# Kernel optimization log

Measured on AMD Instinct MI355X. Metric: run time of the kernel, lower is better.

Reference implementation:

```python
import jax, jax.numpy as jnp
import numpy as np

N = 50000        # nodes
E = 1600000      # edges (avg degree 32)
CZ = 64          # c_z pair channel dim
STEPS = 3        # num_equilibration_steps
DITHER = 1e-4    # dither_eps in average_rotations


def quat_mul(a, b):
    # Hamilton product, quats as [w, x, y, z]
    aw, ax, ay, az = a[..., 0], a[..., 1], a[..., 2], a[..., 3]
    bw, bx, by, bz = b[..., 0], b[..., 1], b[..., 2], b[..., 3]
    return jnp.stack([
        aw * bw - ax * bx - ay * by - az * bz,
        aw * bx + ax * bw + ay * bz - az * by,
        aw * by - ax * bz + ay * bw + az * bx,
        aw * bz + ax * by - ay * bx + az * bw,
    ], axis=-1)


def quat_conj(q):
    return q * jnp.array([1.0, -1.0, -1.0, -1.0], q.dtype)


def quat_to_rot(q):
    w, x, y, z = q[..., 0], q[..., 1], q[..., 2], q[..., 3]
    r00 = 1 - 2 * (y * y + z * z); r01 = 2 * (x * y - w * z); r02 = 2 * (x * z + w * y)
    r10 = 2 * (x * y + w * z); r11 = 1 - 2 * (x * x + z * z); r12 = 2 * (y * z - w * x)
    r20 = 2 * (x * z - w * y); r21 = 2 * (y * z + w * x); r22 = 1 - 2 * (x * x + y * y)
    return jnp.stack([
        jnp.stack([r00, r01, r02], -1),
        jnp.stack([r10, r11, r12], -1),
        jnp.stack([r20, r21, r22], -1),
    ], axis=-2)


def rotmat_to_quat(R):
    # Branchless Shepperd method: 4 candidates, pick numerically best.
    m00, m01, m02 = R[..., 0, 0], R[..., 0, 1], R[..., 0, 2]
    m10, m11, m12 = R[..., 1, 0], R[..., 1, 1], R[..., 1, 2]
    m20, m21, m22 = R[..., 2, 0], R[..., 2, 1], R[..., 2, 2]
    q0 = jnp.stack([1 + m00 + m11 + m22, m21 - m12, m02 - m20, m10 - m01], -1)
    q1 = jnp.stack([m21 - m12, 1 + m00 - m11 - m22, m01 + m10, m02 + m20], -1)
    q2 = jnp.stack([m02 - m20, m01 + m10, 1 - m00 + m11 - m22, m12 + m21], -1)
    q3 = jnp.stack([m10 - m01, m02 + m20, m12 + m21, 1 - m00 - m11 + m22], -1)
    cand = jnp.stack([q0, q1, q2, q3], axis=-2)           # [N,4,4]
    scores = jnp.stack([m00 + m11 + m22, m00, m11, m22], -1)
    idx = jnp.argmax(scores, axis=-1)
    q = cand[jnp.arange(cand.shape[0]), idx]              # [N,4]
    q = q / jnp.linalg.norm(q, axis=-1, keepdims=True)
    return q * jnp.where(q[..., :1] < 0, -1.0, 1.0)      # canonical w >= 0


def rotmat_to_rotvec(R):
    q = rotmat_to_quat(R)
    w, v = q[..., 0], q[..., 1:]
    vn = jnp.linalg.norm(v, axis=-1)
    theta = 2.0 * jnp.arctan2(vn, w)
    small = vn < 1e-6
    safe = jnp.where(small, 1.0, vn)
    return jnp.where(small[..., None], 2.0 * v, (theta / safe)[..., None] * v)


def rotvec_to_quat(rotvec, eps=1e-8):
    theta = jnp.linalg.norm(rotvec + eps, axis=-1)
    omega = rotvec / theta[..., None]
    return jnp.concatenate([jnp.cos(theta / 2)[..., None],
                            jnp.sin(theta / 2)[..., None] * omega], axis=-1)


def setup_inputs() -> dict:
    key = jax.random.key(0)
    ks = jax.random.split(key, 8)
    return {
        "edge_features": jax.random.normal(ks[0], (E, CZ), jnp.float32),
        "quats": jax.random.normal(ks[1], (N, 4), jnp.float32),
        "trans": jax.random.normal(ks[2], (N, 3), jnp.float32) * 10.0,
        "W_update": jax.random.normal(ks[3], (CZ, 6), jnp.float32) * 0.02,
        "b_update": jax.random.normal(ks[4], (6,), jnp.float32) * 0.02,
        "W_logits": jax.random.normal(ks[5], (CZ, 1), jnp.float32) * 0.1,
        "b_logits": jax.random.normal(ks[6], (1,), jnp.float32) * 0.1,
        "edge_index": jax.random.randint(ks[7], (2, E), 0, N, jnp.int32),
    }


def reference(edge_features, quats, trans, W_update, b_update, W_logits, b_logits, edge_index):
    n = quats.shape[0]
    dst, src = edge_index[0], edge_index[1]

    # pairwise update vec + segment softmax weights over destination node (edge_index[1])
    q_upd = edge_features @ W_update + b_update              # [E,6]
    logits = edge_features @ W_logits + b_logits             # [E,1]
    seg_max = jax.ops.segment_max(logits, src, num_segments=n)
    seg_max = jnp.where(jnp.isfinite(seg_max), seg_max, 0.0)
    ex = jnp.exp(logits - seg_max[src])
    denom = jax.ops.segment_sum(ex, src, num_segments=n)
    weights = ex / (denom[src] + 1e-16)                      # [E,1]

    # relative rigid: inv(dst) o src
    qn = quats / jnp.linalg.norm(quats, axis=-1, keepdims=True)
    Rn = quat_to_rot(qn)                                     # [N,3,3]
    q_rel = quat_mul(quat_conj(qn[dst]), qn[src])            # [E,4]
    t_rel = jnp.einsum('eji,ej->ei', Rn[dst], trans[src] - trans[dst])  # R^T (t_s - t_d)

    # compose_q_update_vec (openfold): q' = q + q*(0,b,c,d), normalized; t' = t + R(q) t_vec
    bcd, tvec = q_upd[:, :3], q_upd[:, 3:]
    pair_q = q_rel + quat_mul(q_rel, jnp.concatenate([jnp.zeros_like(bcd[:, :1]), bcd], -1))
    pair_q = pair_q / jnp.linalg.norm(pair_q, axis=-1, keepdims=True)
    pair_t = t_rel + jnp.einsum('eij,ej->ei', quat_to_rot(q_rel), tvec)
    pair_R = quat_to_rot(pair_q)                             # [E,3,3]

    # equilibrate loop: scatter rotation averaging with SVD projection
    R, t = Rn, trans
    key = jax.random.key(42)
    for step in range(STEPS):
        dst_R, dst_t = R[dst], t[dst]
        R_pred = jnp.einsum('eij,ejk->eik', dst_R, pair_R)   # [E,3,3]
        R_sum = jax.ops.segment_sum((R_pred * weights[:, :, None]).reshape(-1, 9),
                                    src, num_segments=n).reshape(n, 3, 3)
        R_sum = R_sum + DITHER * jax.random.normal(jax.random.fold_in(key, step),
                                                   R_sum.shape, R_sum.dtype)
        U, S, Vh = jnp.linalg.svd(R_sum, full_matrices=False)
        d = jnp.linalg.det(U @ Vh)
        col = jnp.stack([jnp.ones_like(d), jnp.ones_like(d), d], -1)[:, None, :]
        R = U @ (Vh * col)                                   # proper rotation
        t_pred = dst_t + jnp.einsum('eij,ej->ei', dst_R, pair_t)
        t = jax.ops.segment_sum(t_pred * weights, src, num_segments=n)

    q_out = rotvec_to_quat(rotmat_to_rotvec(R))
    return jnp.concatenate([q_out, t], axis=-1)              # [N,7]
```

## Files before the change

### kernel.cpp

```cpp
#include <hip/hip_runtime.h>
#include <math.h>

#define TPB 256
#define SCAN_B 1024

__device__ __forceinline__ void quat_to_R(float w, float x, float y, float z, float* R) {
    R[0] = 1.f - 2.f*(y*y + z*z);
    R[1] = 2.f*(x*y - w*z);
    R[2] = 2.f*(x*z + w*y);
    R[3] = 2.f*(x*y + w*z);
    R[4] = 1.f - 2.f*(x*x + z*z);
    R[5] = 2.f*(y*z - w*x);
    R[6] = 2.f*(x*z - w*y);
    R[7] = 2.f*(y*z + w*x);
    R[8] = 1.f - 2.f*(x*x + y*y);
}

__device__ __forceinline__ float hsum32(float v) {
    #pragma unroll
    for (int o = 16; o > 0; o >>= 1) v += __shfl_xor(v, o);
    return v;
}
__device__ __forceinline__ float hmax32(float v) {
    #pragma unroll
    for (int o = 16; o > 0; o >>= 1) v = fmaxf(v, __shfl_xor(v, o));
    return v;
}

__global__ __launch_bounds__(TPB) void k_init(
    const float* __restrict__ quats, const float* __restrict__ trans,
    float* __restrict__ qn, float* __restrict__ RT, int* __restrict__ deg, int N)
{
    int n = blockIdx.x * TPB + threadIdx.x;
    if (n >= N) return;
    float4 q = ((const float4*)quats)[n];
    float inv = rsqrtf(q.x*q.x + q.y*q.y + q.z*q.z + q.w*q.w);
    float w = q.x*inv, x = q.y*inv, y = q.z*inv, z = q.w*inv;
    ((float4*)qn)[n] = make_float4(w, x, y, z);
    float R[9];
    quat_to_R(w, x, y, z, R);
    float t0 = trans[(size_t)n*3+0], t1 = trans[(size_t)n*3+1], t2 = trans[(size_t)n*3+2];
    float4* rt = (float4*)(RT + (size_t)n*12);
    rt[0] = make_float4(R[0], R[1], R[2], t0);
    rt[1] = make_float4(R[3], R[4], R[5], t1);
    rt[2] = make_float4(R[6], R[7], R[8], t2);
    deg[n] = 0;
}

__global__ __launch_bounds__(TPB) void k_hist(
    const int* __restrict__ ei, int* __restrict__ deg, int E)
{
    int e = blockIdx.x * TPB + threadIdx.x;
    if (e >= E) return;
    atomicAdd(deg + ei[(size_t)E + e], 1);
}

__global__ __launch_bounds__(SCAN_B) void k_scan1(
    const int* __restrict__ deg, int* __restrict__ row, int* __restrict__ bsum, int N)
{
    __shared__ int sh[SCAN_B];
    int i = blockIdx.x * SCAN_B + threadIdx.x;
    int v = (i < N) ? deg[i] : 0;
    sh[threadIdx.x] = v;
    __syncthreads();
    #pragma unroll
    for (int o = 1; o < SCAN_B; o <<= 1) {
        int t = (threadIdx.x >= o) ? sh[threadIdx.x - o] : 0;
        __syncthreads();
        sh[threadIdx.x] += t;
        __syncthreads();
    }
    if (i < N) row[i] = sh[threadIdx.x] - v;
    if (threadIdx.x == SCAN_B - 1) bsum[blockIdx.x] = sh[SCAN_B - 1];
}

__global__ __launch_bounds__(SCAN_B) void k_scan2(int* __restrict__ bsum, int nb)
{
    __shared__ int sh[SCAN_B];
    int v = (threadIdx.x < nb) ? bsum[threadIdx.x] : 0;
    sh[threadIdx.x] = v;
    __syncthreads();
    #pragma unroll
    for (int o = 1; o < SCAN_B; o <<= 1) {
        int t = (threadIdx.x >= o) ? sh[threadIdx.x - o] : 0;
        __syncthreads();
        sh[threadIdx.x] += t;
        __syncthreads();
    }
    if (threadIdx.x < nb) bsum[threadIdx.x] = sh[threadIdx.x] - v;
}

__global__ __launch_bounds__(TPB) void k_scan3(
    int* __restrict__ row, const int* __restrict__ bsum,
    int* __restrict__ cursor, int N, int E)
{
    int i = blockIdx.x * TPB + threadIdx.x;
    if (i >= N) return;
    int v = row[i] + bsum[i >> 10];
    row[i] = v;
    cursor[i] = v;
    if (i == 0) row[N] = E;
}

__global__ __launch_bounds__(TPB) void k_edge_pre(
    const float* __restrict__ ef, const int* __restrict__ ei,
    const float* __restrict__ qn, const float* __restrict__ trans,
    const float* __restrict__ Wu, const float* __restrict__ bu,
    const float* __restrict__ Wl, const float* __restrict__ bl,
    int* __restrict__ cursor, float4* __restrict__ pay, int E)
{
    __shared__ __align__(16) float Ws[7][64];
    for (int i = threadIdx.x; i < 7*64; i += TPB) {
        int j = i >> 6, k = i & 63;
        Ws[j][k] = (j < 6) ? Wu[k*6 + j] : Wl[k];
    }
    __syncthreads();
    int t = blockIdx.x * TPB + threadIdx.x;
    int e = t >> 2, sub = t & 3;
    if (e >= E) return;

    float acc[7] = {0.f,0.f,0.f,0.f,0.f,0.f,0.f};
    const float4* ef4 = (const float4*)(ef + (size_t)e * 64) + sub * 4;
    #pragma unroll
    for (int k = 0; k < 4; ++k) {
        float4 v = ef4[k];
        #pragma unroll
        for (int j = 0; j < 7; ++j) {
            float4 w = ((const float4*)Ws[j])[sub*4 + k];
            acc[j] = fmaf(v.x, w.x, fmaf(v.y, w.y, fmaf(v.z, w.z, fmaf(v.w, w.w, acc[j]))));
        }
    }
    #pragma unroll
    for (int j = 0; j < 7; ++j) {
        acc[j] += __shfl_xor(acc[j], 1);
        acc[j] += __shfl_xor(acc[j], 2);
    }
    if (sub) return;

    #pragma unroll
    for (int j = 0; j < 6; ++j) acc[j] += bu[j];
    acc[6] += bl[0];

    int dst = ei[e];
    int src = ei[(size_t)E + e];
    float4 qd = ((const float4*)qn)[dst];
    float4 qs = ((const float4*)qn)[src];
    float aw = qd.x, ax = -qd.y, ay = -qd.z, az = -qd.w;
    float bw = qs.x, bx = qs.y, by = qs.z, bz = qs.w;
    float rw = aw*bw - ax*bx - ay*by - az*bz;
    float rx = aw*bx + ax*bw + ay*bz - az*by;
    float ry = aw*by - ax*bz + ay*bw + az*bx;
    float rz = aw*bz + ax*by - ay*bx + az*bw;
    float b0 = acc[0], b1 = acc[1], b2 = acc[2];
    float pw = rw - rx*b0 - ry*b1 - rz*b2;
    float px = rx + rw*b0 + ry*b2 - rz*b1;
    float py = ry + rw*b1 - rx*b2 + rz*b0;
    float pz = rz + rw*b2 + rx*b1 - ry*b0;
    float pinv = rsqrtf(pw*pw + px*px + py*py + pz*pz);
    pw *= pinv; px *= pinv; py *= pinv; pz *= pinv;
    float dx = trans[(size_t)src*3+0] - trans[(size_t)dst*3+0];
    float dy = trans[(size_t)src*3+1] - trans[(size_t)dst*3+1];
    float dz = trans[(size_t)src*3+2] - trans[(size_t)dst*3+2];
    float Rd[9];
    quat_to_R(qd.x, qd.y, qd.z, qd.w, Rd);
    float tr0 = Rd[0]*dx + Rd[3]*dy + Rd[6]*dz;
    float tr1 = Rd[1]*dx + Rd[4]*dy + Rd[7]*dz;
    float tr2 = Rd[2]*dx + Rd[5]*dy + Rd[8]*dz;
    float Rr[9];
    quat_to_R(rw, rx, ry, rz, Rr);
    float t3 = acc[3], t4 = acc[4], t5 = acc[5];
    float pt0 = tr0 + Rr[0]*t3 + Rr[1]*t4 + Rr[2]*t5;
    float pt1 = tr1 + Rr[3]*t3 + Rr[4]*t4 + Rr[5]*t5;
    float pt2 = tr2 + Rr[6]*t3 + Rr[7]*t4 + Rr[8]*t5;

    int pos = atomicAdd(cursor + src, 1);
    unsigned ub = (unsigned)dst | (pw < 0.f ? 0x80000000u : 0u);
    pay[2*(size_t)pos+0] = make_float4(px, py, pz, __uint_as_float(ub));
    pay[2*(size_t)pos+1] = make_float4(pt0, pt1, pt2, acc[6]);
}

__global__ __launch_bounds__(TPB) void k_node_softmax(
    const int* __restrict__ row, float4* __restrict__ pay, int N)
{
    int g = blockIdx.x * TPB + threadIdx.x;
    int node = g >> 5;
    int ln = threadIdx.x & 31;
    if (node >= N) return;
    int start = row[node], end = row[node + 1];
    float m = -INFINITY, s = 0.f;
    for (int i = start + ln; i < end; i += 32) {
        float l = pay[2*(size_t)i+1].w;
        float mn = fmaxf(m, l);
        s = s * expf(m - mn) + expf(l - mn);
        m = mn;
    }
    float M = hmax32(m);
    float sadj = (m == -INFINITY) ? 0.f : s * expf(m - M);
    float S = hsum32(sadj);
    float inv = 1.f / (S + 1e-16f);
    for (int i = start + ln; i < end; i += 32) {
        float4 v = pay[2*(size_t)i+1];
        v.w = expf(v.w - M) * inv;
        pay[2*(size_t)i+1] = v;
    }
}

__global__ __launch_bounds__(TPB) void k_node_iter(
    const int* __restrict__ row, const float4* __restrict__ pay,
    const float* __restrict__ RT, float* __restrict__ RS, int N)
{
    int g = blockIdx.x * TPB + threadIdx.x;
    int node = g >> 5;
    int ln = threadIdx.x & 31;
    if (node >= N) return;
    int start = row[node], end = row[node + 1];

    float a00=0,a01=0,a02=0,a10=0,a11=0,a12=0,a20=0,a21=0,a22=0,s0=0,s1=0,s2=0;
    for (int i = start + ln; i < end; i += 32) {
        float4 q  = pay[2*(size_t)i+0];
        float4 tl = pay[2*(size_t)i+1];
        unsigned ub = __float_as_uint(q.w);
        int dst = (int)(ub & 0x7fffffffu);
        float s2q = q.x*q.x + q.y*q.y + q.z*q.z;
        float pw = sqrtf(fmaxf(0.f, 1.f - s2q));
        if (ub & 0x80000000u) pw = -pw;
        float w = tl.w;
        float P[9];
        quat_to_R(pw, q.x, q.y, q.z, P);
        const float4* rt = (const float4*)(RT + (size_t)dst * 12);
        float4 r0 = rt[0], r1 = rt[1], r2 = rt[2];
        a00 += w * (r0.x*P[0] + r0.y*P[3] + r0.z*P[6]);
        a01 += w * (r0.x*P[1] + r0.y*P[4] + r0.z*P[7]);
        a02 += w * (r0.x*P[2] + r0.y*P[5] + r0.z*P[8]);
        a10 += w * (r1.x*P[0] + r1.y*P[3] + r1.z*P[6]);
        a11 += w * (r1.x*P[1] + r1.y*P[4] + r1.z*P[7]);
        a12 += w * (r1.x*P[2] + r1.y*P[5] + r1.z*P[8]);
        a20 += w * (r2.x*P[0] + r2.y*P[3] + r2.z*P[6]);
        a21 += w * (r2.x*P[1] + r2.y*P[4] + r2.z*P[7]);
        a22 += w * (r2.x*P[2] + r2.y*P[5] + r2.z*P[8]);
        s0 += w * (r0.w + r0.x*tl.x + r0.y*tl.y + r0.z*tl.z);
        s1 += w * (r1.w + r1.x*tl.x + r1.y*tl.y + r1.z*tl.z);
        s2 += w * (r2.w + r2.x*tl.x + r2.y*tl.y + r2.z*tl.z);
    }
    a00 = hsum32(a00); a01 = hsum32(a01); a02 = hsum32(a02);
    a10 = hsum32(a10); a11 = hsum32(a11); a12 = hsum32(a12);
    a20 = hsum32(a20); a21 = hsum32(a21); a22 = hsum32(a22);
    s0 = hsum32(s0); s1 = hsum32(s1); s2 = hsum32(s2);
    if (ln == 0) {
        float4* rs = (float4*)(RS + (size_t)node * 12);
        rs[0] = make_float4(a00, a01, a02, s0);
        rs[1] = make_float4(a10, a11, a12, s1);
        rs[2] = make_float4(a20, a21, a22, s2);
    }
}

#define JROT(SPP,SQQ,SPQ,SPR,SQR, VP0,VP1,VP2, VQ0,VQ1,VQ2) do { \
    float apq_ = SPQ; \
    if (fabsf(apq_) > 1e-30f) { \
        float tau_ = (SQQ - SPP) / (2.0f * apq_); \
        float tt_ = copysignf(1.0f, tau_) / (fabsf(tau_) + sqrtf(1.0f + tau_*tau_)); \
        float c_ = 1.0f / sqrtf(1.0f + tt_*tt_); \
        float s_ = tt_ * c_; \
        SPP -= tt_ * apq_; SQQ += tt_ * apq_; SPQ = 0.0f; \
        float pr_ = SPR, qr_ = SQR; \
        SPR = c_*pr_ - s_*qr_; SQR = s_*pr_ + c_*qr_; \
        float a_, b_; \
        a_ = VP0; b_ = VQ0; VP0 = c_*a_ - s_*b_; VQ0 = s_*a_ + c_*b_; \
        a_ = VP1; b_ = VQ1; VP1 = c_*a_ - s_*b_; VQ1 = s_*a_ + c_*b_; \
        a_ = VP2; b_ = VQ2; VP2 = c_*a_ - s_*b_; VQ2 = s_*a_ + c_*b_; \
    } \
} while (0)

#define CSW(LA,LB, A0,A1,A2, B0,B1,B2) do { \
    if (LB > LA) { float t_; \
        t_=LA; LA=LB; LB=t_; \
        t_=A0; A0=B0; B0=t_; \
        t_=A1; A1=B1; B1=t_; \
        t_=A2; A2=B2; B2=t_; } \
} while (0)

__global__ __launch_bounds__(TPB) void k_node_project(
    float* __restrict__ RT, const float* __restrict__ RS, int N)
{
    int n = blockIdx.x * TPB + threadIdx.x;
    if (n >= N) return;
    const float4* rs = (const float4*)(RS + (size_t)n * 12);
    float4 q0 = rs[0], q1 = rs[1], q2 = rs[2];
    float A[9] = {q0.x, q0.y, q0.z, q1.x, q1.y, q1.z, q2.x, q2.y, q2.z};
    float t0 = q0.w, t1 = q1.w, t2 = q2.w;

    float s00 = A[0]*A[0] + A[3]*A[3] + A[6]*A[6];
    float s11 = A[1]*A[1] + A[4]*A[4] + A[7]*A[7];
    float s22 = A[2]*A[2] + A[5]*A[5] + A[8]*A[8];
    float s01 = A[0]*A[1] + A[3]*A[4] + A[6]*A[7];
    float s02 = A[0]*A[2] + A[3]*A[5] + A[6]*A[8];
    float s12 = A[1]*A[2] + A[4]*A[5] + A[7]*A[8];
    float v00=1.f,v01=0.f,v02=0.f, v10=0.f,v11=1.f,v12=0.f, v20=0.f,v21=0.f,v22=1.f;
    #pragma unroll
    for (int sweep = 0; sweep < 8; ++sweep) {
        JROT(s00,s11,s01, s02,s12, v00,v10,v20, v01,v11,v21);
        JROT(s00,s22,s02, s01,s12, v00,v10,v20, v02,v12,v22);
        JROT(s11,s22,s12, s01,s02, v01,v11,v21, v02,v12,v22);
    }
    CSW(s00,s11, v00,v10,v20, v01,v11,v21);
    CSW(s00,s22, v00,v10,v20, v02,v12,v22);
    CSW(s11,s22, v01,v11,v21, v02,v12,v22);

    float u0x = A[0]*v00 + A[1]*v10 + A[2]*v20;
    float u0y = A[3]*v00 + A[4]*v10 + A[5]*v20;
    float u0z = A[6]*v00 + A[7]*v10 + A[8]*v20;
    float n0 = sqrtf(u0x*u0x + u0y*u0y + u0z*u0z);
    if (n0 > 1e-20f) { float r = 1.0f/n0; u0x*=r; u0y*=r; u0z*=r; }
    else { u0x = 1.f; u0y = 0.f; u0z = 0.f; }
    float u1x = A[0]*v01 + A[1]*v11 + A[2]*v21;
    float u1y = A[3]*v01 + A[4]*v11 + A[5]*v21;
    float u1z = A[6]*v01 + A[7]*v11 + A[8]*v21;
    float d01 = u1x*u0x + u1y*u0y + u1z*u0z;
    u1x -= d01*u0x; u1y -= d01*u0y; u1z -= d01*u0z;
    float n1 = sqrtf(u1x*u1x + u1y*u1y + u1z*u1z);
    if (n1 > 1e-12f) { float r = 1.0f/n1; u1x*=r; u1y*=r; u1z*=r; }
    else {
        float hx = (fabsf(u0x) < 0.9f) ? 1.f : 0.f;
        float hy = 1.f - hx;
        float cx = -u0z*hy, cy = u0z*hx, cz = u0x*hy - u0y*hx;
        float cn = rsqrtf(cx*cx + cy*cy + cz*cz);
        u1x = cx*cn; u1y = cy*cn; u1z = cz*cn;
    }
    float u2x = u0y*u1z - u0z*u1y;
    float u2y = u0z*u1x - u0x*u1z;
    float u2z = u0x*u1y - u0y*u1x;
    float detV = v00*(v11*v22 - v12*v21) - v01*(v10*v22 - v12*v20) + v02*(v10*v21 - v11*v20);
    if (detV < 0.f) { v02 = -v02; v12 = -v12; v22 = -v22; }
    float4* rt = (float4*)(RT + (size_t)n * 12);
    rt[0] = make_float4(u0x*v00 + u1x*v01 + u2x*v02,
                        u0x*v10 + u1x*v11 + u2x*v12,
                        u0x*v20 + u1x*v21 + u2x*v22, t0);
    rt[1] = make_float4(u0y*v00 + u1y*v01 + u2y*v02,
                        u0y*v10 + u1y*v11 + u2y*v12,
                        u0y*v20 + u1y*v21 + u2y*v22, t1);
    rt[2] = make_float4(u0z*v00 + u1z*v01 + u2z*v02,
                        u0z*v10 + u1z*v11 + u2z*v12,
                        u0z*v20 + u1z*v21 + u2z*v22, t2);
}

__global__ __launch_bounds__(TPB) void k_finalize(
    const float* __restrict__ RT, float* __restrict__ out, int N)
{
    int n = blockIdx.x * TPB + threadIdx.x;
    if (n >= N) return;
    const float4* rt = (const float4*)(RT + (size_t)n * 12);
    float4 r0 = rt[0], r1 = rt[1], r2 = rt[2];
    float m00 = r0.x, m01 = r0.y, m02 = r0.z;
    float m10 = r1.x, m11 = r1.y, m12 = r1.z;
    float m20 = r2.x, m21 = r2.y, m22 = r2.z;
    float tr = m00 + m11 + m22;
    int idx = 0; float best = tr;
    if (m00 > best) { best = m00; idx = 1; }
    if (m11 > best) { best = m11; idx = 2; }
    if (m22 > best) { best = m22; idx = 3; }
    float qw, qx, qy, qz;
    if (idx == 0)      { qw = 1.f+m00+m11+m22; qx = m21-m12;        qy = m02-m20;        qz = m10-m01; }
    else if (idx == 1) { qw = m21-m12;         qx = 1.f+m00-m11-m22; qy = m01+m10;       qz = m02+m20; }
    else if (idx == 2) { qw = m02-m20;         qx = m01+m10;        qy = 1.f-m00+m11-m22; qz = m12+m21; }
    else               { qw = m10-m01;         qx = m02+m20;        qy = m12+m21;        qz = 1.f-m00-m11+m22; }
    float inv = rsqrtf(qw*qw + qx*qx + qy*qy + qz*qz);
    qw *= inv; qx *= inv; qy *= inv; qz *= inv;
    if (qw < 0.f) { qw = -qw; qx = -qx; qy = -qy; qz = -qz; }
    float vn = sqrtf(qx*qx + qy*qy + qz*qz);
    float theta = 2.f * atan2f(vn, qw);
    float r0v, r1v, r2v;
    if (vn < 1e-6f) { r0v = 2.f*qx; r1v = 2.f*qy; r2v = 2.f*qz; }
    else { float s = theta / vn; r0v = s*qx; r1v = s*qy; r2v = s*qz; }
    float e0 = r0v + 1e-8f, e1 = r1v + 1e-8f, e2 = r2v + 1e-8f;
    float th2 = sqrtf(e0*e0 + e1*e1 + e2*e2);
    float half = 0.5f * th2;
    float cw = cosf(half), sw = sinf(half);
    float it = 1.0f / th2;
    out[(size_t)n*7+0] = cw;
    out[(size_t)n*7+1] = sw * r0v * it;
    out[(size_t)n*7+2] = sw * r1v * it;
    out[(size_t)n*7+3] = sw * r2v * it;
    out[(size_t)n*7+4] = r0.w;
    out[(size_t)n*7+5] = r1.w;
    out[(size_t)n*7+6] = r2.w;
}

extern "C" void kernel_launch(void* const* d_in, const int* in_sizes, int n_in,
                              void* d_out, int out_size, void* d_ws, size_t ws_size,
                              hipStream_t stream)
{
    (void)n_in; (void)out_size; (void)ws_size;
    const float* ef    = (const float*)d_in[0];
    const float* quats = (const float*)d_in[1];
    const float* trans = (const float*)d_in[2];
    const float* Wu    = (const float*)d_in[3];
    const float* bu    = (const float*)d_in[4];
    const float* Wl    = (const float*)d_in[5];
    const float* bl    = (const float*)d_in[6];
    const int*   ei    = (const int*)d_in[7];
    float* out = (float*)d_out;

    const int N = in_sizes[1] / 4;
    const int E = in_sizes[7] / 2;

    float* ws = (float*)d_ws;
    size_t off = 0;
    float*  qn   = ws + off; off += (size_t)4*N;
    float4* pay  = (float4*)(ws + off); off += (size_t)8*E;
    float*  RT   = ws + off; off += (size_t)12*N;
    float*  RS   = ws + off; off += (size_t)12*N;
    int* deg    = (int*)(ws + off); off += (size_t)N;
    int* row    = (int*)(ws + off); off += (size_t)(N + 1);
    int* bsum   = (int*)(ws + off); off += (size_t)SCAN_B;

    int nodeBlocks = (N + TPB - 1) / TPB;
    int edgeBlocks = (E + TPB - 1) / TPB;
    int edge4Blocks = (int)(((size_t)4*E + TPB - 1) / TPB);
    int halfBlocks = (int)(((size_t)N * 32 + TPB - 1) / TPB);
    int scanBlocks = (N + SCAN_B - 1) / SCAN_B;

    k_init<<<nodeBlocks, TPB, 0, stream>>>(quats, trans, qn, RT, deg, N);
    k_hist<<<edgeBlocks, TPB, 0, stream>>>(ei, deg, E);
    k_scan1<<<scanBlocks, SCAN_B, 0, stream>>>(deg, row, bsum, N);
    k_scan2<<<1, SCAN_B, 0, stream>>>(bsum, scanBlocks);
    k_scan3<<<nodeBlocks, TPB, 0, stream>>>(row, bsum, deg, N, E);
    k_edge_pre<<<edge4Blocks, TPB, 0, stream>>>(ef, ei, qn, trans, Wu, bu, Wl, bl,
                                                deg, pay, E);
    k_node_softmax<<<halfBlocks, TPB, 0, stream>>>(row, pay, N);
    for (int s = 0; s < 3; ++s) {
        k_node_iter<<<halfBlocks, TPB, 0, stream>>>(row, pay, RT, RS, N);
        k_node_project<<<nodeBlocks, TPB, 0, stream>>>(RT, RS, N);
    }
    k_finalize<<<nodeBlocks, TPB, 0, stream>>>(RT, out, N);
}
```

Baseline: 365.3 us.

## Decouple CSR scatter from edge precompute via index permutation and gather in softmax

Edge precompute now writes its 32-byte payload in edge order, and a separate kernel builds a CSR permutation index with atomics. The softmax kernel gathers the payloads through that index and writes them CSR-ordered into a second buffer. This removes the scattered atomic-position writes from the heavy edge kernel so its stores are coalesced. In exchange it adds an extra kernel, an extra full payload copy (read plus write of about 51 MB) and an E-sized index buffer.

After: 495.1 us. 35.5% more time.

```diff
diff --git a/kernel.cpp b/kernel.cpp
--- a/kernel.cpp
+++ b/kernel.cpp
@@ -102,12 +102,22 @@
     if (i == 0) row[N] = E;
 }
 
+__global__ __launch_bounds__(TPB) void k_scatter_idx(
+    const int* __restrict__ ei, int* __restrict__ cursor, int* __restrict__ idx, int E)
+{
+    int e = blockIdx.x * TPB + threadIdx.x;
+    if (e >= E) return;
+    int src = ei[(size_t)E + e];
+    int pos = atomicAdd(cursor + src, 1);
+    idx[pos] = e;
+}
+
 __global__ __launch_bounds__(TPB) void k_edge_pre(
     const float* __restrict__ ef, const int* __restrict__ ei,
     const float* __restrict__ qn, const float* __restrict__ trans,
     const float* __restrict__ Wu, const float* __restrict__ bu,
     const float* __restrict__ Wl, const float* __restrict__ bl,
-    int* __restrict__ cursor, float4* __restrict__ pay, int E)
+    float4* __restrict__ payE, int E)
 {
     __shared__ __align__(16) float Ws[7][64];
     for (int i = threadIdx.x; i < 7*64; i += TPB) {
@@ -173,23 +183,25 @@
     float pt1 = tr1 + Rr[3]*t3 + Rr[4]*t4 + Rr[5]*t5;
     float pt2 = tr2 + Rr[6]*t3 + Rr[7]*t4 + Rr[8]*t5;
 
-    int pos = atomicAdd(cursor + src, 1);
     unsigned ub = (unsigned)dst | (pw < 0.f ? 0x80000000u : 0u);
-    pay[2*(size_t)pos+0] = make_float4(px, py, pz, __uint_as_float(ub));
-    pay[2*(size_t)pos+1] = make_float4(pt0, pt1, pt2, acc[6]);
+    payE[2*(size_t)e+0] = make_float4(px, py, pz, __uint_as_float(ub));
+    payE[2*(size_t)e+1] = make_float4(pt0, pt1, pt2, acc[6]);
 }
 
 __global__ __launch_bounds__(TPB) void k_node_softmax(
-    const int* __restrict__ row, float4* __restrict__ pay, int N)
+    const int* __restrict__ row, const int* __restrict__ idx,
+    const float4* __restrict__ payE, float4* __restrict__ payC, int N)
 {
     int g = blockIdx.x * TPB + threadIdx.x;
     int node = g >> 5;
     int ln = threadIdx.x & 31;
     if (node >= N) return;
     int start = row[node], end = row[node + 1];
+    const float* pf = (const float*)payE;
     float m = -INFINITY, s = 0.f;
     for (int i = start + ln; i < end; i += 32) {
-        float l = pay[2*(size_t)i+1].w;
+        int e = idx[i];
+        float l = pf[8*(size_t)e + 7];
         float mn = fmaxf(m, l);
         s = s * expf(m - mn) + expf(l - mn);
         m = mn;
@@ -199,14 +211,17 @@
     float S = hsum32(sadj);
     float inv = 1.f / (S + 1e-16f);
     for (int i = start + ln; i < end; i += 32) {
-        float4 v = pay[2*(size_t)i+1];
-        v.w = expf(v.w - M) * inv;
-        pay[2*(size_t)i+1] = v;
+        int e = idx[i];
+        float4 a = payE[2*(size_t)e+0];
+        float4 b = payE[2*(size_t)e+1];
+        b.w = expf(b.w - M) * inv;
+        payC[2*(size_t)i+0] = a;
+        payC[2*(size_t)i+1] = b;
     }
 }
 
 __global__ __launch_bounds__(TPB) void k_node_iter(
-    const int* __restrict__ row, const float4* __restrict__ pay,
+    const int* __restrict__ row, const float4* __restrict__ payC,
     const float* __restrict__ RT, float* __restrict__ RS, int N)
 {
     int g = blockIdx.x * TPB + threadIdx.x;
@@ -217,8 +232,8 @@
 
     float a00=0,a01=0,a02=0,a10=0,a11=0,a12=0,a20=0,a21=0,a22=0,s0=0,s1=0,s2=0;
     for (int i = start + ln; i < end; i += 32) {
-        float4 q  = pay[2*(size_t)i+0];
-        float4 tl = pay[2*(size_t)i+1];
+        float4 q  = payC[2*(size_t)i+0];
+        float4 tl = payC[2*(size_t)i+1];
         unsigned ub = __float_as_uint(q.w);
         int dst = (int)(ub & 0x7fffffffu);
         float s2q = q.x*q.x + q.y*q.y + q.z*q.z;
@@ -406,12 +421,14 @@
     float* ws = (float*)d_ws;
     size_t off = 0;
     float*  qn   = ws + off; off += (size_t)4*N;
-    float4* pay  = (float4*)(ws + off); off += (size_t)8*E;
+    float4* payE = (float4*)(ws + off); off += (size_t)8*E;
+    float4* payC = (float4*)(ws + off); off += (size_t)8*E;
     float*  RT   = ws + off; off += (size_t)12*N;
     float*  RS   = ws + off; off += (size_t)12*N;
     int* deg    = (int*)(ws + off); off += (size_t)N;
     int* row    = (int*)(ws + off); off += (size_t)(N + 1);
     int* bsum   = (int*)(ws + off); off += (size_t)SCAN_B;
+    int* idx    = (int*)(ws + off); off += (size_t)E;
 
     int nodeBlocks = (N + TPB - 1) / TPB;
     int edgeBlocks = (E + TPB - 1) / TPB;
@@ -424,11 +441,12 @@
     k_scan1<<<scanBlocks, SCAN_B, 0, stream>>>(deg, row, bsum, N);
     k_scan2<<<1, SCAN_B, 0, stream>>>(bsum, scanBlocks);
     k_scan3<<<nodeBlocks, TPB, 0, stream>>>(row, bsum, deg, N, E);
+    k_scatter_idx<<<edgeBlocks, TPB, 0, stream>>>(ei, deg, idx, E);
     k_edge_pre<<<edge4Blocks, TPB, 0, stream>>>(ef, ei, qn, trans, Wu, bu, Wl, bl,
-                                                deg, pay, E);
-    k_node_softmax<<<halfBlocks, TPB, 0, stream>>>(row, pay, N);
+                                                payE, E);
+    k_node_softmax<<<halfBlocks, TPB, 0, stream>>>(row, idx, payE, payC, N);
     for (int s = 0; s < 3; ++s) {
-        k_node_iter<<<halfBlocks, TPB, 0, stream>>>(row, pay, RT, RS, N);
+        k_node_iter<<<halfBlocks, TPB, 0, stream>>>(row, payC, RT, RS, N);
         k_node_project<<<nodeBlocks, TPB, 0, stream>>>(RT, RS, N);
     }
     k_finalize<<<nodeBlocks, TPB, 0, stream>>>(RT, out, N);
```

## Split edge GEMV from geometry kernel and interleave edge feature loads

Applied to the files above, without the earlier changes.

Splits the fused edge preprocessing kernel into a 4-threads-per-edge projection kernel writing two float4 intermediates, and a 1-thread-per-edge geometry kernel that does quaternion math, the cursor atomic, and payload scatter. The feature load pattern changes so the four sub-threads read adjacent float4s, improving coalescing. Previously 3 of 4 lanes idled during geometry. The cost is an extra kernel launch and a round trip of 32 bytes per edge through global memory.

Result: slower. 389.1 us (+6.5%).

```diff
diff --git a/kernel.cpp b/kernel.cpp
--- a/kernel.cpp
+++ b/kernel.cpp
@@ -102,12 +102,11 @@
     if (i == 0) row[N] = E;
 }
 
-__global__ __launch_bounds__(TPB) void k_edge_pre(
-    const float* __restrict__ ef, const int* __restrict__ ei,
-    const float* __restrict__ qn, const float* __restrict__ trans,
+__global__ __launch_bounds__(TPB) void k_gemm(
+    const float* __restrict__ ef,
     const float* __restrict__ Wu, const float* __restrict__ bu,
     const float* __restrict__ Wl, const float* __restrict__ bl,
-    int* __restrict__ cursor, float4* __restrict__ pay, int E)
+    float4* __restrict__ qa, float4* __restrict__ qb, int E)
 {
     __shared__ __align__(16) float Ws[7][64];
     for (int i = threadIdx.x; i < 7*64; i += TPB) {
@@ -120,13 +119,13 @@
     if (e >= E) return;
 
     float acc[7] = {0.f,0.f,0.f,0.f,0.f,0.f,0.f};
-    const float4* ef4 = (const float4*)(ef + (size_t)e * 64) + sub * 4;
+    const float4* ef4 = (const float4*)(ef + (size_t)e * 64);
     #pragma unroll
     for (int k = 0; k < 4; ++k) {
-        float4 v = ef4[k];
+        float4 v = ef4[sub + 4*k];
         #pragma unroll
         for (int j = 0; j < 7; ++j) {
-            float4 w = ((const float4*)Ws[j])[sub*4 + k];
+            float4 w = ((const float4*)Ws[j])[sub + 4*k];
             acc[j] = fmaf(v.x, w.x, fmaf(v.y, w.y, fmaf(v.z, w.z, fmaf(v.w, w.w, acc[j]))));
         }
     }
@@ -136,11 +135,20 @@
         acc[j] += __shfl_xor(acc[j], 2);
     }
     if (sub) return;
-
-    #pragma unroll
-    for (int j = 0; j < 6; ++j) acc[j] += bu[j];
-    acc[6] += bl[0];
-
+    qa[e] = make_float4(acc[0] + bu[0], acc[1] + bu[1], acc[2] + bu[2], acc[6] + bl[0]);
+    qb[e] = make_float4(acc[3] + bu[3], acc[4] + bu[4], acc[5] + bu[5], 0.f);
+}
+
+__global__ __launch_bounds__(TPB) void k_geom(
+    const int* __restrict__ ei, const float* __restrict__ qn,
+    const float* __restrict__ trans,
+    const float4* __restrict__ qa, const float4* __restrict__ qb,
+    int* __restrict__ cursor, float4* __restrict__ pay, int E)
+{
+    int e = blockIdx.x * TPB + threadIdx.x;
+    if (e >= E) return;
+    float4 A = qa[e];
+    float4 B = qb[e];
     int dst = ei[e];
     int src = ei[(size_t)E + e];
     float4 qd = ((const float4*)qn)[dst];
@@ -151,7 +159,7 @@
     float rx = aw*bx + ax*bw + ay*bz - az*by;
     float ry = aw*by - ax*bz + ay*bw + az*bx;
     float rz = aw*bz + ax*by - ay*bx + az*bw;
-    float b0 = acc[0], b1 = acc[1], b2 = acc[2];
+    float b0 = A.x, b1 = A.y, b2 = A.z;
     float pw = rw - rx*b0 - ry*b1 - rz*b2;
     float px = rx + rw*b0 + ry*b2 - rz*b1;
     float py = ry + rw*b1 - rx*b2 + rz*b0;
@@ -168,15 +176,14 @@
     float tr2 = Rd[2]*dx + Rd[5]*dy + Rd[8]*dz;
     float Rr[9];
     quat_to_R(rw, rx, ry, rz, Rr);
-    float t3 = acc[3], t4 = acc[4], t5 = acc[5];
-    float pt0 = tr0 + Rr[0]*t3 + Rr[1]*t4 + Rr[2]*t5;
-    float pt1 = tr1 + Rr[3]*t3 + Rr[4]*t4 + Rr[5]*t5;
-    float pt2 = tr2 + Rr[6]*t3 + Rr[7]*t4 + Rr[8]*t5;
+    float pt0 = tr0 + Rr[0]*B.x + Rr[1]*B.y + Rr[2]*B.z;
+    float pt1 = tr1 + Rr[3]*B.x + Rr[4]*B.y + Rr[5]*B.z;
+    float pt2 = tr2 + Rr[6]*B.x + Rr[7]*B.y + Rr[8]*B.z;
 
     int pos = atomicAdd(cursor + src, 1);
     unsigned ub = (unsigned)dst | (pw < 0.f ? 0x80000000u : 0u);
     pay[2*(size_t)pos+0] = make_float4(px, py, pz, __uint_as_float(ub));
-    pay[2*(size_t)pos+1] = make_float4(pt0, pt1, pt2, acc[6]);
+    pay[2*(size_t)pos+1] = make_float4(pt0, pt1, pt2, A.w);
 }
 
 __global__ __launch_bounds__(TPB) void k_node_softmax(
@@ -407,6 +414,8 @@
     size_t off = 0;
     float*  qn   = ws + off; off += (size_t)4*N;
     float4* pay  = (float4*)(ws + off); off += (size_t)8*E;
+    float4* qa   = (float4*)(ws + off); off += (size_t)4*E;
+    float4* qb   = (float4*)(ws + off); off += (size_t)4*E;
     float*  RT   = ws + off; off += (size_t)12*N;
     float*  RS   = ws + off; off += (size_t)12*N;
     int* deg    = (int*)(ws + off); off += (size_t)N;
@@ -424,8 +433,8 @@
     k_scan1<<<scanBlocks, SCAN_B, 0, stream>>>(deg, row, bsum, N);
     k_scan2<<<1, SCAN_B, 0, stream>>>(bsum, scanBlocks);
     k_scan3<<<nodeBlocks, TPB, 0, stream>>>(row, bsum, deg, N, E);
-    k_edge_pre<<<edge4Blocks, TPB, 0, stream>>>(ef, ei, qn, trans, Wu, bu, Wl, bl,
-                                                deg, pay, E);
+    k_gemm<<<edge4Blocks, TPB, 0, stream>>>(ef, Wu, bu, Wl, bl, qa, qb, E);
+    k_geom<<<edgeBlocks, TPB, 0, stream>>>(ei, qn, trans, qa, qb, deg, pay, E);
     k_node_softmax<<<halfBlocks, TPB, 0, stream>>>(row, pay, N);
     for (int s = 0; s < 3; ++s) {
         k_node_iter<<<halfBlocks, TPB, 0, stream>>>(row, pay, RT, RS, N);
```

## Fuse SVD projection and finalize into node iteration, precompute CSR ranks

Applied to the files above, without the earlier changes.

Merges the per-node SVD projection and the final quaternion conversion into the gather-reduce kernel. It ping-pongs between two RT buffers, which removes four launches and the round trip through the RS buffer. The histogram pass now records each edge's rank from its atomic, so the edge pre-pass computes its CSR position without a second atomic on a cursor. The edge epilogue is also split across two lanes: one writes the rotation payload and the other the translation payload. In exchange, the Jacobi SVD now runs on lane 0 of each 32-lane group, so most lanes idle during the projection, and an extra E-sized rank buffer is written and read.

Result: slower. 477.7 us (+30.8%).

```diff
diff --git a/kernel.cpp b/kernel.cpp
--- a/kernel.cpp
+++ b/kernel.cpp
@@ -48,11 +48,11 @@
 }
 
 __global__ __launch_bounds__(TPB) void k_hist(
-    const int* __restrict__ ei, int* __restrict__ deg, int E)
+    const int* __restrict__ ei, int* __restrict__ deg, int* __restrict__ rank, int E)
 {
     int e = blockIdx.x * TPB + threadIdx.x;
     if (e >= E) return;
-    atomicAdd(deg + ei[(size_t)E + e], 1);
+    rank[e] = atomicAdd(deg + ei[(size_t)E + e], 1);
 }
 
 __global__ __launch_bounds__(SCAN_B) void k_scan1(
@@ -91,14 +91,11 @@
 }
 
 __global__ __launch_bounds__(TPB) void k_scan3(
-    int* __restrict__ row, const int* __restrict__ bsum,
-    int* __restrict__ cursor, int N, int E)
+    int* __restrict__ row, const int* __restrict__ bsum, int N, int E)
 {
     int i = blockIdx.x * TPB + threadIdx.x;
     if (i >= N) return;
-    int v = row[i] + bsum[i >> 10];
-    row[i] = v;
-    cursor[i] = v;
+    row[i] = row[i] + bsum[i >> 10];
     if (i == 0) row[N] = E;
 }
 
@@ -107,7 +104,8 @@
     const float* __restrict__ qn, const float* __restrict__ trans,
     const float* __restrict__ Wu, const float* __restrict__ bu,
     const float* __restrict__ Wl, const float* __restrict__ bl,
-    int* __restrict__ cursor, float4* __restrict__ pay, int E)
+    const int* __restrict__ row, const int* __restrict__ rank,
+    float4* __restrict__ pay, int E)
 {
     __shared__ __align__(16) float Ws[7][64];
     for (int i = threadIdx.x; i < 7*64; i += TPB) {
@@ -135,11 +133,7 @@
         acc[j] += __shfl_xor(acc[j], 1);
         acc[j] += __shfl_xor(acc[j], 2);
     }
-    if (sub) return;
-
-    #pragma unroll
-    for (int j = 0; j < 6; ++j) acc[j] += bu[j];
-    acc[6] += bl[0];
+    if (sub > 1) return;
 
     int dst = ei[e];
     int src = ei[(size_t)E + e];
@@ -151,32 +145,35 @@
     float rx = aw*bx + ax*bw + ay*bz - az*by;
     float ry = aw*by - ax*bz + ay*bw + az*bx;
     float rz = aw*bz + ax*by - ay*bx + az*bw;
-    float b0 = acc[0], b1 = acc[1], b2 = acc[2];
-    float pw = rw - rx*b0 - ry*b1 - rz*b2;
-    float px = rx + rw*b0 + ry*b2 - rz*b1;
-    float py = ry + rw*b1 - rx*b2 + rz*b0;
-    float pz = rz + rw*b2 + rx*b1 - ry*b0;
-    float pinv = rsqrtf(pw*pw + px*px + py*py + pz*pz);
-    pw *= pinv; px *= pinv; py *= pinv; pz *= pinv;
-    float dx = trans[(size_t)src*3+0] - trans[(size_t)dst*3+0];
-    float dy = trans[(size_t)src*3+1] - trans[(size_t)dst*3+1];
-    float dz = trans[(size_t)src*3+2] - trans[(size_t)dst*3+2];
-    float Rd[9];
-    quat_to_R(qd.x, qd.y, qd.z, qd.w, Rd);
-    float tr0 = Rd[0]*dx + Rd[3]*dy + Rd[6]*dz;
-    float tr1 = Rd[1]*dx + Rd[4]*dy + Rd[7]*dz;
-    float tr2 = Rd[2]*dx + Rd[5]*dy + Rd[8]*dz;
-    float Rr[9];
-    quat_to_R(rw, rx, ry, rz, Rr);
-    float t3 = acc[3], t4 = acc[4], t5 = acc[5];
-    float pt0 = tr0 + Rr[0]*t3 + Rr[1]*t4 + Rr[2]*t5;
-    float pt1 = tr1 + Rr[3]*t3 + Rr[4]*t4 + Rr[5]*t5;
-    float pt2 = tr2 + Rr[6]*t3 + Rr[7]*t4 + Rr[8]*t5;
-
-    int pos = atomicAdd(cursor + src, 1);
-    unsigned ub = (unsigned)dst | (pw < 0.f ? 0x80000000u : 0u);
-    pay[2*(size_t)pos+0] = make_float4(px, py, pz, __uint_as_float(ub));
-    pay[2*(size_t)pos+1] = make_float4(pt0, pt1, pt2, acc[6]);
+    int pos = row[src] + rank[e];
+
+    if (sub == 0) {
+        float b0 = acc[0] + bu[0], b1 = acc[1] + bu[1], b2 = acc[2] + bu[2];
+        float pw = rw - rx*b0 - ry*b1 - rz*b2;
+        float px = rx + rw*b0 + ry*b2 - rz*b1;
+        float py = ry + rw*b1 - rx*b2 + rz*b0;
+        float pz = rz + rw*b2 + rx*b1 - ry*b0;
+        float pinv = rsqrtf(pw*pw + px*px + py*py + pz*pz);
+        px *= pinv; py *= pinv; pz *= pinv;
+        unsigned ub = (unsigned)dst | (pw < 0.f ? 0x80000000u : 0u);
+        pay[2*(size_t)pos+0] = make_float4(px, py, pz, __uint_as_float(ub));
+    } else {
+        float dx = trans[(size_t)src*3+0] - trans[(size_t)dst*3+0];
+        float dy = trans[(size_t)src*3+1] - trans[(size_t)dst*3+1];
+        float dz = trans[(size_t)src*3+2] - trans[(size_t)dst*3+2];
+        float Rd[9];
+        quat_to_R(qd.x, qd.y, qd.z, qd.w, Rd);
+        float tr0 = Rd[0]*dx + Rd[3]*dy + Rd[6]*dz;
+        float tr1 = Rd[1]*dx + Rd[4]*dy + Rd[7]*dz;
+        float tr2 = Rd[2]*dx + Rd[5]*dy + Rd[8]*dz;
+        float Rr[9];
+        quat_to_R(rw, rx, ry, rz, Rr);
+        float t3 = acc[3] + bu[3], t4 = acc[4] + bu[4], t5 = acc[5] + bu[5];
+        float pt0 = tr0 + Rr[0]*t3 + Rr[1]*t4 + Rr[2]*t5;
+        float pt1 = tr1 + Rr[3]*t3 + Rr[4]*t4 + Rr[5]*t5;
+        float pt2 = tr2 + Rr[6]*t3 + Rr[7]*t4 + Rr[8]*t5;
+        pay[2*(size_t)pos+1] = make_float4(pt0, pt1, pt2, acc[6] + bl[0]);
+    }
 }
 
 __global__ __launch_bounds__(TPB) void k_node_softmax(
@@ -202,55 +199,6 @@
         float4 v = pay[2*(size_t)i+1];
         v.w = expf(v.w - M) * inv;
         pay[2*(size_t)i+1] = v;
-    }
-}
-
-__global__ __launch_bounds__(TPB) void k_node_iter(
-    const int* __restrict__ row, const float4* __restrict__ pay,
-    const float* __restrict__ RT, float* __restrict__ RS, int N)
-{
-    int g = blockIdx.x * TPB + threadIdx.x;
-    int node = g >> 5;
-    int ln = threadIdx.x & 31;
-    if (node >= N) return;
-    int start = row[node], end = row[node + 1];
-
-    float a00=0,a01=0,a02=0,a10=0,a11=0,a12=0,a20=0,a21=0,a22=0,s0=0,s1=0,s2=0;
-    for (int i = start + ln; i < end; i += 32) {
-        float4 q  = pay[2*(size_t)i+0];
-        float4 tl = pay[2*(size_t)i+1];
-        unsigned ub = __float_as_uint(q.w);
-        int dst = (int)(ub & 0x7fffffffu);
-        float s2q = q.x*q.x + q.y*q.y + q.z*q.z;
-        float pw = sqrtf(fmaxf(0.f, 1.f - s2q));
-        if (ub & 0x80000000u) pw = -pw;
-        float w = tl.w;
-        float P[9];
-        quat_to_R(pw, q.x, q.y, q.z, P);
-        const float4* rt = (const float4*)(RT + (size_t)dst * 12);
-        float4 r0 = rt[0], r1 = rt[1], r2 = rt[2];
-        a00 += w * (r0.x*P[0] + r0.y*P[3] + r0.z*P[6]);
-        a01 += w * (r0.x*P[1] + r0.y*P[4] + r0.z*P[7]);
-        a02 += w * (r0.x*P[2] + r0.y*P[5] + r0.z*P[8]);
-        a10 += w * (r1.x*P[0] + r1.y*P[3] + r1.z*P[6]);
-        a11 += w * (r1.x*P[1] + r1.y*P[4] + r1.z*P[7]);
-        a12 += w * (r1.x*P[2] + r1.y*P[5] + r1.z*P[8]);
-        a20 += w * (r2.x*P[0] + r2.y*P[3] + r2.z*P[6]);
-        a21 += w * (r2.x*P[1] + r2.y*P[4] + r2.z*P[7]);
-        a22 += w * (r2.x*P[2] + r2.y*P[5] + r2.z*P[8]);
-        s0 += w * (r0.w + r0.x*tl.x + r0.y*tl.y + r0.z*tl.z);
-        s1 += w * (r1.w + r1.x*tl.x + r1.y*tl.y + r1.z*tl.z);
-        s2 += w * (r2.w + r2.x*tl.x + r2.y*tl.y + r2.z*tl.z);
-    }
-    a00 = hsum32(a00); a01 = hsum32(a01); a02 = hsum32(a02);
-    a10 = hsum32(a10); a11 = hsum32(a11); a12 = hsum32(a12);
-    a20 = hsum32(a20); a21 = hsum32(a21); a22 = hsum32(a22);
-    s0 = hsum32(s0); s1 = hsum32(s1); s2 = hsum32(s2);
-    if (ln == 0) {
-        float4* rs = (float4*)(RS + (size_t)node * 12);
-        rs[0] = make_float4(a00, a01, a02, s0);
-        rs[1] = make_float4(a10, a11, a12, s1);
-        rs[2] = make_float4(a20, a21, a22, s2);
     }
 }
 
@@ -279,32 +227,67 @@
         t_=A2; A2=B2; B2=t_; } \
 } while (0)
 
-__global__ __launch_bounds__(TPB) void k_node_project(
-    float* __restrict__ RT, const float* __restrict__ RS, int N)
-{
-    int n = blockIdx.x * TPB + threadIdx.x;
-    if (n >= N) return;
-    const float4* rs = (const float4*)(RS + (size_t)n * 12);
-    float4 q0 = rs[0], q1 = rs[1], q2 = rs[2];
-    float A[9] = {q0.x, q0.y, q0.z, q1.x, q1.y, q1.z, q2.x, q2.y, q2.z};
-    float t0 = q0.w, t1 = q1.w, t2 = q2.w;
-
-    float s00 = A[0]*A[0] + A[3]*A[3] + A[6]*A[6];
-    float s11 = A[1]*A[1] + A[4]*A[4] + A[7]*A[7];
-    float s22 = A[2]*A[2] + A[5]*A[5] + A[8]*A[8];
-    float s01 = A[0]*A[1] + A[3]*A[4] + A[6]*A[7];
-    float s02 = A[0]*A[2] + A[3]*A[5] + A[6]*A[8];
-    float s12 = A[1]*A[2] + A[4]*A[5] + A[7]*A[8];
+__global__ __launch_bounds__(TPB) void k_node_iter(
+    const int* __restrict__ row, const float4* __restrict__ pay,
+    const float* __restrict__ RT_in, float* __restrict__ RT_out,
+    float* __restrict__ outp, int write_out, int N)
+{
+    int g = blockIdx.x * TPB + threadIdx.x;
+    int node = g >> 5;
+    int ln = threadIdx.x & 31;
+    if (node >= N) return;
+    int start = row[node], end = row[node + 1];
+
+    float a00=0,a01=0,a02=0,a10=0,a11=0,a12=0,a20=0,a21=0,a22=0,s0=0,s1=0,s2=0;
+    for (int i = start + ln; i < end; i += 32) {
+        float4 q  = pay[2*(size_t)i+0];
+        float4 tl = pay[2*(size_t)i+1];
+        unsigned ub = __float_as_uint(q.w);
+        int dst = (int)(ub & 0x7fffffffu);
+        float s2q = q.x*q.x + q.y*q.y + q.z*q.z;
+        float pw = sqrtf(fmaxf(0.f, 1.f - s2q));
+        if (ub & 0x80000000u) pw = -pw;
+        float w = tl.w;
+        float P[9];
+        quat_to_R(pw, q.x, q.y, q.z, P);
+        const float4* rt = (const float4*)(RT_in + (size_t)dst * 12);
+        float4 r0 = rt[0], r1 = rt[1], r2 = rt[2];
+        a00 += w * (r0.x*P[0] + r0.y*P[3] + r0.z*P[6]);
+        a01 += w * (r0.x*P[1] + r0.y*P[4] + r0.z*P[7]);
+        a02 += w * (r0.x*P[2] + r0.y*P[5] + r0.z*P[8]);
+        a10 += w * (r1.x*P[0] + r1.y*P[3] + r1.z*P[6]);
+        a11 += w * (r1.x*P[1] + r1.y*P[4] + r1.z*P[7]);
+        a12 += w * (r1.x*P[2] + r1.y*P[5] + r1.z*P[8]);
+        a20 += w * (r2.x*P[0] + r2.y*P[3] + r2.z*P[6]);
+        a21 += w * (r2.x*P[1] + r2.y*P[4] + r2.z*P[7]);
+        a22 += w * (r2.x*P[2] + r2.y*P[5] + r2.z*P[8]);
+        s0 += w * (r0.w + r0.x*tl.x + r0.y*tl.y + r0.z*tl.z);
+        s1 += w * (r1.w + r1.x*tl.x + r1.y*tl.y + r1.z*tl.z);
+        s2 += w * (r2.w + r2.x*tl.x + r2.y*tl.y + r2.z*tl.z);
+    }
+    a00 = hsum32(a00); a01 = hsum32(a01); a02 = hsum32(a02);
+    a10 = hsum32(a10); a11 = hsum32(a11); a12 = hsum32(a12);
+    a20 = hsum32(a20); a21 = hsum32(a21); a22 = hsum32(a22);
+    s0 = hsum32(s0); s1 = hsum32(s1); s2 = hsum32(s2);
+    if (ln != 0) return;
+
+    float A[9] = {a00, a01, a02, a10, a11, a12, a20, a21, a22};
+    float q00 = A[0]*A[0] + A[3]*A[3] + A[6]*A[6];
+    float q11 = A[1]*A[1] + A[4]*A[4] + A[7]*A[7];
+    float q22 = A[2]*A[2] + A[5]*A[5] + A[8]*A[8];
+    float q01 = A[0]*A[1] + A[3]*A[4] + A[6]*A[7];
+    float q02 = A[0]*A[2] + A[3]*A[5] + A[6]*A[8];
+    float q12 = A[1]*A[2] + A[4]*A[5] + A[7]*A[8];
     float v00=1.f,v01=0.f,v02=0.f, v10=0.f,v11=1.f,v12=0.f, v20=0.f,v21=0.f,v22=1.f;
     #pragma unroll
     for (int sweep = 0; sweep < 8; ++sweep) {
-        JROT(s00,s11,s01, s02,s12, v00,v10,v20, v01,v11,v21);
-        JROT(s00,s22,s02, s01,s12, v00,v10,v20, v02,v12,v22);
-        JROT(s11,s22,s12, s01,s02, v01,v11,v21, v02,v12,v22);
-    }
-    CSW(s00,s11, v00,v10,v20, v01,v11,v21);
-    CSW(s00,s22, v00,v10,v20, v02,v12,v22);
-    CSW(s11,s22, v01,v11,v21, v02,v12,v22);
+        JROT(q00,q11,q01, q02,q12, v00,v10,v20, v01,v11,v21);
+        JROT(q00,q22,q02, q01,q12, v00,v10,v20, v02,v12,v22);
+        JROT(q11,q22,q12, q01,q02, v01,v11,v21, v02,v12,v22);
+    }
+    CSW(q00,q11, v00,v10,v20, v01,v11,v21);
+    CSW(q00,q22, v00,v10,v20, v02,v12,v22);
+    CSW(q11,q22, v01,v11,v21, v02,v12,v22);
 
     float u0x = A[0]*v00 + A[1]*v10 + A[2]*v20;
     float u0y = A[3]*v00 + A[4]*v10 + A[5]*v20;
@@ -331,28 +314,21 @@
     float u2z = u0x*u1y - u0y*u1x;
     float detV = v00*(v11*v22 - v12*v21) - v01*(v10*v22 - v12*v20) + v02*(v10*v21 - v11*v20);
     if (detV < 0.f) { v02 = -v02; v12 = -v12; v22 = -v22; }
-    float4* rt = (float4*)(RT + (size_t)n * 12);
-    rt[0] = make_float4(u0x*v00 + u1x*v01 + u2x*v02,
-                        u0x*v10 + u1x*v11 + u2x*v12,
-                        u0x*v20 + u1x*v21 + u2x*v22, t0);
-    rt[1] = make_float4(u0y*v00 + u1y*v01 + u2y*v02,
-                        u0y*v10 + u1y*v11 + u2y*v12,
-                        u0y*v20 + u1y*v21 + u2y*v22, t1);
-    rt[2] = make_float4(u0z*v00 + u1z*v01 + u2z*v02,
-                        u0z*v10 + u1z*v11 + u2z*v12,
-                        u0z*v20 + u1z*v21 + u2z*v22, t2);
-}
-
-__global__ __launch_bounds__(TPB) void k_finalize(
-    const float* __restrict__ RT, float* __restrict__ out, int N)
-{
-    int n = blockIdx.x * TPB + threadIdx.x;
-    if (n >= N) return;
-    const float4* rt = (const float4*)(RT + (size_t)n * 12);
-    float4 r0 = rt[0], r1 = rt[1], r2 = rt[2];
-    float m00 = r0.x, m01 = r0.y, m02 = r0.z;
-    float m10 = r1.x, m11 = r1.y, m12 = r1.z;
-    float m20 = r2.x, m21 = r2.y, m22 = r2.z;
+    float m00 = u0x*v00 + u1x*v01 + u2x*v02;
+    float m01 = u0x*v10 + u1x*v11 + u2x*v12;
+    float m02 = u0x*v20 + u1x*v21 + u2x*v22;
+    float m10 = u0y*v00 + u1y*v01 + u2y*v02;
+    float m11 = u0y*v10 + u1y*v11 + u2y*v12;
+    float m12 = u0y*v20 + u1y*v21 + u2y*v22;
+    float m20 = u0z*v00 + u1z*v01 + u2z*v02;
+    float m21 = u0z*v10 + u1z*v11 + u2z*v12;
+    float m22 = u0z*v20 + u1z*v21 + u2z*v22;
+    float4* rt = (float4*)(RT_out + (size_t)node * 12);
+    rt[0] = make_float4(m00, m01, m02, s0);
+    rt[1] = make_float4(m10, m11, m12, s1);
+    rt[2] = make_float4(m20, m21, m22, s2);
+
+    if (!write_out) return;
     float tr = m00 + m11 + m22;
     int idx = 0; float best = tr;
     if (m00 > best) { best = m00; idx = 1; }
@@ -376,13 +352,13 @@
     float half = 0.5f * th2;
     float cw = cosf(half), sw = sinf(half);
     float it = 1.0f / th2;
-    out[(size_t)n*7+0] = cw;
-    out[(size_t)n*7+1] = sw * r0v * it;
-    out[(size_t)n*7+2] = sw * r1v * it;
-    out[(size_t)n*7+3] = sw * r2v * it;
-    out[(size_t)n*7+4] = r0.w;
-    out[(size_t)n*7+5] = r1.w;
-    out[(size_t)n*7+6] = r2.w;
+    outp[(size_t)node*7+0] = cw;
+    outp[(size_t)node*7+1] = sw * r0v * it;
+    outp[(size_t)node*7+2] = sw * r1v * it;
+    outp[(size_t)node*7+3] = sw * r2v * it;
+    outp[(size_t)node*7+4] = s0;
+    outp[(size_t)node*7+5] = s1;
+    outp[(size_t)node*7+6] = s2;
 }
 
 extern "C" void kernel_launch(void* const* d_in, const int* in_sizes, int n_in,
@@ -407,11 +383,12 @@
     size_t off = 0;
     float*  qn   = ws + off; off += (size_t)4*N;
     float4* pay  = (float4*)(ws + off); off += (size_t)8*E;
-    float*  RT   = ws + off; off += (size_t)12*N;
-    float*  RS   = ws + off; off += (size_t)12*N;
+    float*  RT0  = ws + off; off += (size_t)12*N;
+    float*  RT1  = ws + off; off += (size_t)12*N;
     int* deg    = (int*)(ws + off); off += (size_t)N;
     int* row    = (int*)(ws + off); off += (size_t)(N + 1);
     int* bsum   = (int*)(ws + off); off += (size_t)SCAN_B;
+    int* rank   = (int*)(ws + off); off += (size_t)E;
 
     int nodeBlocks = (N + TPB - 1) / TPB;
     int edgeBlocks = (E + TPB - 1) / TPB;
@@ -419,17 +396,15 @@
     int halfBlocks = (int)(((size_t)N * 32 + TPB - 1) / TPB);
     int scanBlocks = (N + SCAN_B - 1) / SCAN_B;
 
-    k_init<<<nodeBlocks, TPB, 0, stream>>>(quats, trans, qn, RT, deg, N);
-    k_hist<<<edgeBlocks, TPB, 0, stream>>>(ei, deg, E);
+    k_init<<<nodeBlocks, TPB, 0, stream>>>(quats, trans, qn, RT0, deg, N);
+    k_hist<<<edgeBlocks, TPB, 0, stream>>>(ei, deg, rank, E);
     k_scan1<<<scanBlocks, SCAN_B, 0, stream>>>(deg, row, bsum, N);
     k_scan2<<<1, SCAN_B, 0, stream>>>(bsum, scanBlocks);
-    k_scan3<<<nodeBlocks, TPB, 0, stream>>>(row, bsum, deg, N, E);
+    k_scan3<<<nodeBlocks, TPB, 0, stream>>>(row, bsum, N, E);
     k_edge_pre<<<edge4Blocks, TPB, 0, stream>>>(ef, ei, qn, trans, Wu, bu, Wl, bl,
-                                                deg, pay, E);
+                                                row, rank, pay, E);
     k_node_softmax<<<halfBlocks, TPB, 0, stream>>>(row, pay, N);
-    for (int s = 0; s < 3; ++s) {
-        k_node_iter<<<halfBlocks, TPB, 0, stream>>>(row, pay, RT, RS, N);
-        k_node_project<<<nodeBlocks, TPB, 0, stream>>>(RT, RS, N);
-    }
-    k_finalize<<<nodeBlocks, TPB, 0, stream>>>(RT, out, N);
-}
+    k_node_iter<<<halfBlocks, TPB, 0, stream>>>(row, pay, RT0, RT1, out, 0, N);
+    k_node_iter<<<halfBlocks, TPB, 0, stream>>>(row, pay, RT1, RT0, out, 0, N);
+    k_node_iter<<<halfBlocks, TPB, 0, stream>>>(row, pay, RT0, RT1, out, 1, N);
+}
```
